# Kernel tuning notes

Measured on AMD Instinct MI355X. Metric: run time of the kernel, lower is better.

## Reference

```python
import jax, jax.numpy as jnp
import numpy as np
from jax.experimental.ode import odeint

RN = 10000   # number of radial grid points (para['rn'])
RM = 200.0   # max radius (para['rm'])
NE = 1000    # number of eigenvalue samples (evl_tr)


def setup_inputs() -> dict:
    # Match the source driver exactly: evl = linspace(-0.05, 1, 1000),
    # r_dsc = linspace(rm/rn, rm, rn).
    evl = jnp.linspace(-0.05, 1.0, NE, dtype=jnp.float32)
    r_dsc = jnp.linspace(RM / RN, RM, RN, dtype=jnp.float32)
    return {"evl": evl, "r_dsc": r_dsc}


def reference(evl, r_dsc):
    E = evl.shape[0]
    # init state: rad = 0, rad' = 1  -> shape [E, 2]
    y0 = jnp.stack([jnp.zeros((E,), evl.dtype), jnp.ones((E,), evl.dtype)], axis=-1)

    def ode_func(y, t, evl):
        rad = y[:, 0]
        rad_d = y[:, 1]
        # ptl_rs = -2/r (Coulomb potential term), broadcast over eigenvalues
        rad_dd = (-2.0 / t - evl) * rad
        return jnp.stack([rad_d, rad_dd], axis=-1)

    # dopri5 adaptive RK45, same tolerances as torchdiffeq call.
    # Output: [RN, E, 2] solution sampled at every r_dsc point.
    return odeint(ode_func, y0, r_dsc, evl, rtol=1e-6, atol=1e-9)
```

## Files before the change

kernel.cpp:

```cpp
#include <hip/hip_runtime.h>

#define NE_  1000
#define RN_  10000
#define NI_  (RN_ - 1)
#define CH_  10
#define NCH_ 1000
#define GL_  25
#define GG_  40

__device__ __forceinline__ float rcpf(float x) { return __builtin_amdgcn_rcpf(x); }

__device__ __forceinline__ void substeps_for(int p, int& S, float& invS) {
    if (p < 16)      { S = 4; invS = 0.25f; }
    else if (p < 64) { S = 2; invS = 0.5f;  }
    else             { S = 1; invS = 1.0f;  }
}

template <int NV>
__device__ __forceinline__ void rk4_step(float q1, float q2, float q3,
                                         float h2, float h, float h6,
                                         float a[NV], float b[NV]) {
#pragma unroll
    for (int v = 0; v < NV; ++v) {
        const float ya = a[v], yb = b[v];
        const float k1a = yb;                const float k1b = q1 * ya;
        const float y2a = fmaf(h2, k1a, ya); const float y2b = fmaf(h2, k1b, yb);
        const float k2a = y2b;               const float k2b = q2 * y2a;
        const float y3a = fmaf(h2, k2a, ya); const float y3b = fmaf(h2, k2b, yb);
        const float k3a = y3b;               const float k3b = q2 * y3a;
        const float y4a = fmaf(h,  k3a, ya); const float y4b = fmaf(h,  k3b, yb);
        const float k4a = y4b;               const float k4b = q3 * y4a;
        a[v] = fmaf(h6, fmaf(2.0f, k2a + k3a, k1a + k4a), ya);
        b[v] = fmaf(h6, fmaf(2.0f, k2b + k3b, k1b + k4b), yb);
    }
}

template <int NV>
__device__ __forceinline__ void advance_interval(float ta, float tb, float e,
                                                 int S, float invS,
                                                 float a[NV], float b[NV]) {
    const float hs = (tb - ta) * invS;
    const float h2 = 0.5f * hs;
    const float h6 = hs * (1.0f / 6.0f);
    for (int j = 0; j < S; ++j) {
        const float t0 = ta + hs * (float)j;
        const float q1 = fmaf(-2.0f, rcpf(t0),      -e);
        const float q2 = fmaf(-2.0f, rcpf(t0 + h2), -e);
        const float q3 = fmaf(-2.0f, rcpf(t0 + hs), -e);
        rk4_step<NV>(q1, q2, q3, h2, hs, h6, a, b);
    }
}

__global__ void k_prop(const float* __restrict__ evl, const float* __restrict__ t,
                       float4* __restrict__ M) {
    const int tid = blockIdx.x * blockDim.x + threadIdx.x;
    if (tid >= NE_ * NCH_) return;
    const int ei = tid % NE_;
    const int c  = tid / NE_;
    const float e    = evl[ei];
    const float t0g  = t[0];
    const float step = (t[RN_ - 1] - t0g) * (1.0f / (float)NI_);
    const int p0 = c * CH_;
    const int p1 = min(p0 + CH_, NI_);
    float a[2] = {1.0f, 0.0f};
    float b[2] = {0.0f, 1.0f};
    if (p0 >= 64 && p0 + CH_ == p1) {
        float tcur = fmaf((float)p0, step, t0g);
        float qcur = fmaf(-2.0f, rcpf(tcur), -e);
#pragma unroll
        for (int k = 0; k < CH_ / 2; ++k) {
            const float pf    = (float)(p0 + 2 * k);
            const float tmid  = fmaf(pf + 1.0f, step, t0g);
            const float tnext = fmaf(pf + 2.0f, step, t0g);
            const float h  = tnext - tcur;
            const float h2 = 0.5f * h;
            const float h6 = h * (1.0f / 6.0f);
            const float qmid  = fmaf(-2.0f, rcpf(tmid),  -e);
            const float qnext = fmaf(-2.0f, rcpf(tnext), -e);
            rk4_step<2>(qcur, qmid, qnext, h2, h, h6, a, b);
            tcur = tnext; qcur = qnext;
        }
    } else {
        for (int p = p0; p < p1; ++p) {
            const float ta = fmaf((float)p,       step, t0g);
            const float tb = fmaf((float)(p + 1), step, t0g);
            int S; float invS; substeps_for(p, S, invS);
            advance_interval<2>(ta, tb, e, S, invS, a, b);
        }
    }
    M[tid] = make_float4(a[0], b[0], a[1], b[1]);
}

__device__ __forceinline__ float4 mmul(float4 B, float4 A) {
    float4 r;
    r.x = fmaf(B.x, A.x, B.z * A.y);
    r.y = fmaf(B.y, A.x, B.w * A.y);
    r.z = fmaf(B.x, A.z, B.z * A.w);
    r.w = fmaf(B.y, A.z, B.w * A.w);
    return r;
}

__global__ void k_group(const float4* __restrict__ M, float4* __restrict__ Mg) {
    const int tid = blockIdx.x * blockDim.x + threadIdx.x;
    if (tid >= NE_ * GG_) return;
    const int ei = tid % NE_;
    const int g  = tid / NE_;
    float4 m[GL_];
#pragma unroll
    for (int k = 0; k < GL_; ++k)
        m[k] = M[(size_t)(g * GL_ + k) * NE_ + ei];
    float4 C = m[0];
#pragma unroll
    for (int k = 1; k < GL_; ++k) C = mmul(m[k], C);
    Mg[(size_t)g * NE_ + ei] = C;
}

__global__ void k_scan_groups(const float4* __restrict__ Mg,
                              float2* __restrict__ Yg) {
    const int ei = blockIdx.x * blockDim.x + threadIdx.x;
    if (ei >= NE_) return;
    float ya = 0.0f, yb = 1.0f;
    for (int g0 = 0; g0 < GG_; g0 += 20) {
        float4 m[20];
#pragma unroll
        for (int k = 0; k < 20; ++k)
            m[k] = Mg[(size_t)(g0 + k) * NE_ + ei];
#pragma unroll
        for (int k = 0; k < 20; ++k) {
            Yg[(size_t)(g0 + k) * NE_ + ei] = make_float2(ya, yb);
            const float na = fmaf(m[k].x, ya, m[k].z * yb);
            const float nb = fmaf(m[k].y, ya, m[k].w * yb);
            ya = na; yb = nb;
        }
    }
}

__global__ void k_expand(const float4* __restrict__ M,
                         const float2* __restrict__ Yg,
                         float2* __restrict__ Yst) {
    const int tid = blockIdx.x * blockDim.x + threadIdx.x;
    if (tid >= NE_ * GG_) return;
    const int ei = tid % NE_;
    const int g  = tid / NE_;
    float4 m[GL_];
#pragma unroll
    for (int k = 0; k < GL_; ++k)
        m[k] = M[(size_t)(g * GL_ + k) * NE_ + ei];
    const float2 y0 = Yg[(size_t)g * NE_ + ei];
    float ya = y0.x, yb = y0.y;
#pragma unroll
    for (int k = 0; k < GL_; ++k) {
        Yst[(size_t)(g * GL_ + k) * NE_ + ei] = make_float2(ya, yb);
        const float na = fmaf(m[k].x, ya, m[k].z * yb);
        const float nb = fmaf(m[k].y, ya, m[k].w * yb);
        ya = na; yb = nb;
    }
}

__global__ void k_out(const float* __restrict__ evl, const float* __restrict__ t,
                      const float2* __restrict__ Yst, float2* __restrict__ out) {
    const int tid = blockIdx.x * blockDim.x + threadIdx.x;
    if (tid >= NE_ * NCH_) return;
    const int ei = tid % NE_;
    const int c  = tid / NE_;
    const float e    = evl[ei];
    const float t0g  = t[0];
    const float step = (t[RN_ - 1] - t0g) * (1.0f / (float)NI_);
    const int p0 = c * CH_;
    const int p1 = min(p0 + CH_, NI_);
    const float2 y0 = Yst[tid];
    float a[1] = {y0.x};
    float b[1] = {y0.y};
    if (c == 0) out[ei] = make_float2(0.0f, 1.0f);
    if (p0 >= 64 && p0 + CH_ == p1) {
        float tcur = fmaf((float)p0, step, t0g);
        float qcur = fmaf(-2.0f, rcpf(tcur), -e);
#pragma unroll
        for (int k = 0; k < CH_; ++k) {
            const float pf    = (float)(p0 + k);
            const float tmid  = fmaf(pf + 0.5f, step, t0g);
            const float tnext = fmaf(pf + 1.0f, step, t0g);
            const float h  = tnext - tcur;
            const float h2 = 0.5f * h;
            const float h6 = h * (1.0f / 6.0f);
            const float qmid  = fmaf(-2.0f, rcpf(tmid),  -e);
            const float qnext = fmaf(-2.0f, rcpf(tnext), -e);
            rk4_step<1>(qcur, qmid, qnext, h2, h, h6, a, b);
            out[(size_t)(p0 + k + 1) * NE_ + ei] = make_float2(a[0], b[0]);
            tcur = tnext; qcur = qnext;
        }
    } else {
        for (int p = p0; p < p1; ++p) {
            const float ta = fmaf((float)p,       step, t0g);
            const float tb = fmaf((float)(p + 1), step, t0g);
            int S; float invS; substeps_for(p, S, invS);
            advance_interval<1>(ta, tb, e, S, invS, a, b);
            out[(size_t)(p + 1) * NE_ + ei] = make_float2(a[0], b[0]);
        }
    }
}

__global__ void k_serial(const float* __restrict__ evl, const float* __restrict__ t,
                         float2* __restrict__ out) {
    const int ei = blockIdx.x * blockDim.x + threadIdx.x;
    if (ei >= NE_) return;
    const float e    = evl[ei];
    const float t0g  = t[0];
    const float step = (t[RN_ - 1] - t0g) * (1.0f / (float)NI_);
    float a[1] = {0.0f};
    float b[1] = {1.0f};
    out[ei] = make_float2(0.0f, 1.0f);
    for (int p = 0; p < NI_; ++p) {
        const float ta = fmaf((float)p,       step, t0g);
        const float tb = fmaf((float)(p + 1), step, t0g);
        int S; float invS; substeps_for(p, S, invS);
        advance_interval<1>(ta, tb, e, S, invS, a, b);
        out[(size_t)(p + 1) * NE_ + ei] = make_float2(a[0], b[0]);
    }
}

extern "C" void kernel_launch(void* const* d_in, const int* in_sizes, int n_in,
                              void* d_out, int out_size, void* d_ws, size_t ws_size,
                              hipStream_t stream) {
    const float* evl = (const float*)d_in[0];
    const float* t   = (const float*)d_in[1];
    float2* out = (float2*)d_out;

    const size_t szM   = (size_t)NCH_ * NE_ * sizeof(float4);
    const size_t szYst = (size_t)NCH_ * NE_ * sizeof(float2);
    const size_t szMg  = (size_t)GG_  * NE_ * sizeof(float4);
    const size_t szYg  = (size_t)GG_  * NE_ * sizeof(float2);

    if (ws_size < szM + szYst + szMg + szYg) {
        k_serial<<<(NE_ + 255) / 256, 256, 0, stream>>>(evl, t, out);
        return;
    }

    char* p = (char*)d_ws;
    float4* M   = (float4*)p;               p += szM;
    float2* Yst = (float2*)p;               p += szYst;
    float4* Mg  = (float4*)p;               p += szMg;
    float2* Yg  = (float2*)p;

    const int ntask   = NE_ * NCH_;
    const int blocks  = (ntask + 255) / 256;
    const int gtask   = NE_ * GG_;
    const int gblocks = (gtask + 255) / 256;

    k_prop<<<blocks, 256, 0, stream>>>(evl, t, M);
    k_group<<<gblocks, 256, 0, stream>>>(M, Mg);
    k_scan_groups<<<4, 256, 0, stream>>>(Mg, Yg);
    k_expand<<<gblocks, 256, 0, stream>>>(M, Yg, Yst);
    k_out<<<blocks, 256, 0, stream>>>(evl, t, Yst, out);
}
```

Baseline: 119.6 us.

## Fuse propagation, group products, scan and expansion into one shared-memory kernel

Replaces four kernels (per-chunk transfer matrices, group products, serial group scan, expansion) with one kernel. Each block handles 8 energies with 64 slots, and each slot computes 16 chunk matrices held in registers. The slot products are scanned in shared memory, and the chunk start states are written straight out. This removes the global round-trip of the full matrix array and three launches. In exchange the kernel uses more registers (16 float4 per thread) and runs a serial 64-step scan in one slot, which may lower occupancy. There are only 125 blocks, which may underfill the GPU.

After: 124.5 us. 4.1% more time.

```diff
diff --git a/kernel.cpp b/kernel.cpp
--- a/kernel.cpp
+++ b/kernel.cpp
@@ -1,12 +1,13 @@
 #include <hip/hip_runtime.h>
 
-#define NE_  1000
-#define RN_  10000
-#define NI_  (RN_ - 1)
-#define CH_  10
-#define NCH_ 1000
-#define GL_  25
-#define GG_  40
+#define NE_    1000
+#define RN_    10000
+#define NI_    (RN_ - 1)
+#define CH_    10
+#define NCH_   1000
+#define SLOTS_ 64
+#define CPS_   16
+#define CPB_   8
 
 __device__ __forceinline__ float rcpf(float x) { return __builtin_amdgcn_rcpf(x); }
 
@@ -51,46 +52,6 @@
     }
 }
 
-__global__ void k_prop(const float* __restrict__ evl, const float* __restrict__ t,
-                       float4* __restrict__ M) {
-    const int tid = blockIdx.x * blockDim.x + threadIdx.x;
-    if (tid >= NE_ * NCH_) return;
-    const int ei = tid % NE_;
-    const int c  = tid / NE_;
-    const float e    = evl[ei];
-    const float t0g  = t[0];
-    const float step = (t[RN_ - 1] - t0g) * (1.0f / (float)NI_);
-    const int p0 = c * CH_;
-    const int p1 = min(p0 + CH_, NI_);
-    float a[2] = {1.0f, 0.0f};
-    float b[2] = {0.0f, 1.0f};
-    if (p0 >= 64 && p0 + CH_ == p1) {
-        float tcur = fmaf((float)p0, step, t0g);
-        float qcur = fmaf(-2.0f, rcpf(tcur), -e);
-#pragma unroll
-        for (int k = 0; k < CH_ / 2; ++k) {
-            const float pf    = (float)(p0 + 2 * k);
-            const float tmid  = fmaf(pf + 1.0f, step, t0g);
-            const float tnext = fmaf(pf + 2.0f, step, t0g);
-            const float h  = tnext - tcur;
-            const float h2 = 0.5f * h;
-            const float h6 = h * (1.0f / 6.0f);
-            const float qmid  = fmaf(-2.0f, rcpf(tmid),  -e);
-            const float qnext = fmaf(-2.0f, rcpf(tnext), -e);
-            rk4_step<2>(qcur, qmid, qnext, h2, h, h6, a, b);
-            tcur = tnext; qcur = qnext;
-        }
-    } else {
-        for (int p = p0; p < p1; ++p) {
-            const float ta = fmaf((float)p,       step, t0g);
-            const float tb = fmaf((float)(p + 1), step, t0g);
-            int S; float invS; substeps_for(p, S, invS);
-            advance_interval<2>(ta, tb, e, S, invS, a, b);
-        }
-    }
-    M[tid] = make_float4(a[0], b[0], a[1], b[1]);
-}
-
 __device__ __forceinline__ float4 mmul(float4 B, float4 A) {
     float4 r;
     r.x = fmaf(B.x, A.x, B.z * A.y);
@@ -100,59 +61,87 @@
     return r;
 }
 
-__global__ void k_group(const float4* __restrict__ M, float4* __restrict__ Mg) {
-    const int tid = blockIdx.x * blockDim.x + threadIdx.x;
-    if (tid >= NE_ * GG_) return;
-    const int ei = tid % NE_;
-    const int g  = tid / NE_;
-    float4 m[GL_];
-#pragma unroll
-    for (int k = 0; k < GL_; ++k)
-        m[k] = M[(size_t)(g * GL_ + k) * NE_ + ei];
-    float4 C = m[0];
-#pragma unroll
-    for (int k = 1; k < GL_; ++k) C = mmul(m[k], C);
-    Mg[(size_t)g * NE_ + ei] = C;
-}
-
-__global__ void k_scan_groups(const float4* __restrict__ Mg,
-                              float2* __restrict__ Yg) {
-    const int ei = blockIdx.x * blockDim.x + threadIdx.x;
-    if (ei >= NE_) return;
-    float ya = 0.0f, yb = 1.0f;
-    for (int g0 = 0; g0 < GG_; g0 += 20) {
-        float4 m[20];
-#pragma unroll
-        for (int k = 0; k < 20; ++k)
-            m[k] = Mg[(size_t)(g0 + k) * NE_ + ei];
-#pragma unroll
-        for (int k = 0; k < 20; ++k) {
-            Yg[(size_t)(g0 + k) * NE_ + ei] = make_float2(ya, yb);
-            const float na = fmaf(m[k].x, ya, m[k].z * yb);
-            const float nb = fmaf(m[k].y, ya, m[k].w * yb);
+__global__ __launch_bounds__(CPB_ * SLOTS_) void
+k_scanfused(const float* __restrict__ evl, const float* __restrict__ t,
+            float2* __restrict__ Yst) {
+    __shared__ float4 lm[CPB_][SLOTS_];
+    __shared__ float2 ly[CPB_][SLOTS_];
+
+    const int tid  = threadIdx.x;
+    const int eil  = tid & (CPB_ - 1);
+    const int slot = tid >> 3;
+    const int ei   = blockIdx.x * CPB_ + eil;
+
+    const float e    = evl[ei];
+    const float t0g  = t[0];
+    const float step = (t[RN_ - 1] - t0g) * (1.0f / (float)NI_);
+
+    float4 Mc[CPS_];
+#pragma unroll
+    for (int i = 0; i < CPS_; ++i) {
+        const int c  = slot * CPS_ + i;
+        const int p0 = c * CH_;
+        const int p1 = min(p0 + CH_, NI_);
+        float a2[2] = {1.0f, 0.0f};
+        float b2[2] = {0.0f, 1.0f};
+        if (p0 < NI_) {
+            if (p0 >= 64 && p1 == p0 + CH_) {
+                float tcur = fmaf((float)p0, step, t0g);
+                float qcur = fmaf(-2.0f, rcpf(tcur), -e);
+#pragma unroll
+                for (int k = 0; k < CH_ / 2; ++k) {
+                    const float pf    = (float)(p0 + 2 * k);
+                    const float tmid  = fmaf(pf + 1.0f, step, t0g);
+                    const float tnext = fmaf(pf + 2.0f, step, t0g);
+                    const float h  = tnext - tcur;
+                    const float h2 = 0.5f * h;
+                    const float h6 = h * (1.0f / 6.0f);
+                    const float qmid  = fmaf(-2.0f, rcpf(tmid),  -e);
+                    const float qnext = fmaf(-2.0f, rcpf(tnext), -e);
+                    rk4_step<2>(qcur, qmid, qnext, h2, h, h6, a2, b2);
+                    tcur = tnext; qcur = qnext;
+                }
+            } else {
+                for (int p = p0; p < p1; ++p) {
+                    const float ta = fmaf((float)p,       step, t0g);
+                    const float tb = fmaf((float)(p + 1), step, t0g);
+                    int S; float invS; substeps_for(p, S, invS);
+                    advance_interval<2>(ta, tb, e, S, invS, a2, b2);
+                }
+            }
+        }
+        Mc[i] = make_float4(a2[0], b2[0], a2[1], b2[1]);
+    }
+
+    float4 C = Mc[0];
+#pragma unroll
+    for (int i = 1; i < CPS_; ++i) C = mmul(Mc[i], C);
+    lm[eil][slot] = C;
+    __syncthreads();
+
+    if (slot == 0) {
+        float ya = 0.0f, yb = 1.0f;
+#pragma unroll 8
+        for (int k = 0; k < SLOTS_; ++k) {
+            ly[eil][k] = make_float2(ya, yb);
+            const float4 m = lm[eil][k];
+            const float na = fmaf(m.x, ya, m.z * yb);
+            const float nb = fmaf(m.y, ya, m.w * yb);
             ya = na; yb = nb;
         }
     }
-}
-
-__global__ void k_expand(const float4* __restrict__ M,
-                         const float2* __restrict__ Yg,
-                         float2* __restrict__ Yst) {
-    const int tid = blockIdx.x * blockDim.x + threadIdx.x;
-    if (tid >= NE_ * GG_) return;
-    const int ei = tid % NE_;
-    const int g  = tid / NE_;
-    float4 m[GL_];
-#pragma unroll
-    for (int k = 0; k < GL_; ++k)
-        m[k] = M[(size_t)(g * GL_ + k) * NE_ + ei];
-    const float2 y0 = Yg[(size_t)g * NE_ + ei];
+    __syncthreads();
+
+    const float2 y0 = ly[eil][slot];
     float ya = y0.x, yb = y0.y;
 #pragma unroll
-    for (int k = 0; k < GL_; ++k) {
-        Yst[(size_t)(g * GL_ + k) * NE_ + ei] = make_float2(ya, yb);
-        const float na = fmaf(m[k].x, ya, m[k].z * yb);
-        const float nb = fmaf(m[k].y, ya, m[k].w * yb);
+    for (int i = 0; i < CPS_; ++i) {
+        const int c = slot * CPS_ + i;
+        if (c < NCH_)
+            Yst[(size_t)c * NE_ + ei] = make_float2(ya, yb);
+        const float4 m = Mc[i];
+        const float na = fmaf(m.x, ya, m.z * yb);
+        const float nb = fmaf(m.y, ya, m.w * yb);
         ya = na; yb = nb;
     }
 }
@@ -226,30 +215,14 @@
     const float* t   = (const float*)d_in[1];
     float2* out = (float2*)d_out;
 
-    const size_t szM   = (size_t)NCH_ * NE_ * sizeof(float4);
-    const size_t szYst = (size_t)NCH_ * NE_ * sizeof(float2);
-    const size_t szMg  = (size_t)GG_  * NE_ * sizeof(float4);
-    const size_t szYg  = (size_t)GG_  * NE_ * sizeof(float2);
-
-    if (ws_size < szM + szYst + szMg + szYg) {
+    const size_t needYst = (size_t)NCH_ * NE_ * sizeof(float2);
+    if (ws_size < needYst) {
         k_serial<<<(NE_ + 255) / 256, 256, 0, stream>>>(evl, t, out);
         return;
     }
-
-    char* p = (char*)d_ws;
-    float4* M   = (float4*)p;               p += szM;
-    float2* Yst = (float2*)p;               p += szYst;
-    float4* Mg  = (float4*)p;               p += szMg;
-    float2* Yg  = (float2*)p;
-
-    const int ntask   = NE_ * NCH_;
-    const int blocks  = (ntask + 255) / 256;
-    const int gtask   = NE_ * GG_;
-    const int gblocks = (gtask + 255) / 256;
-
-    k_prop<<<blocks, 256, 0, stream>>>(evl, t, M);
-    k_group<<<gblocks, 256, 0, stream>>>(M, Mg);
-    k_scan_groups<<<4, 256, 0, stream>>>(Mg, Yg);
-    k_expand<<<gblocks, 256, 0, stream>>>(M, Yg, Yst);
-    k_out<<<blocks, 256, 0, stream>>>(evl, t, Yst, out);
-}
+    float2* Yst = (float2*)d_ws;
+
+    k_scanfused<<<NE_ / CPB_, CPB_ * SLOTS_, 0, stream>>>(evl, t, Yst);
+    const int ntask = NE_ * NCH_;
+    k_out<<<(ntask + 255) / 256, 256, 0, stream>>>(evl, t, Yst, out);
+}
```

## Merge group scan into expand and use wider RK4 steps in prop

Applied to the files above, without the earlier changes.

Removes the single-wave k_scan_groups launch. Each expand thread now recomputes its own group prefix by applying all earlier group matrices directly, which trades one launch and a serial dependency for redundant reads and FMAs of Mg. Separately, the fast path of k_prop now takes three RK4 steps of widths 4, 4 and 2 grid intervals instead of five steps of width 2. This cuts the arithmetic in that path but raises the per-step truncation error, so accuracy may suffer.

New measurement: 117.1 us. 1.02x faster.

```diff
diff --git a/kernel.cpp b/kernel.cpp
--- a/kernel.cpp
+++ b/kernel.cpp
@@ -67,18 +67,20 @@
     if (p0 >= 64 && p0 + CH_ == p1) {
         float tcur = fmaf((float)p0, step, t0g);
         float qcur = fmaf(-2.0f, rcpf(tcur), -e);
-#pragma unroll
-        for (int k = 0; k < CH_ / 2; ++k) {
-            const float pf    = (float)(p0 + 2 * k);
-            const float tmid  = fmaf(pf + 1.0f, step, t0g);
-            const float tnext = fmaf(pf + 2.0f, step, t0g);
+        int p = p0;
+        const int widths[3] = {4, 4, 2};
+#pragma unroll
+        for (int s = 0; s < 3; ++s) {
+            const int w = widths[s];
+            const float tmid  = fmaf((float)(p + w / 2), step, t0g);
+            const float tnext = fmaf((float)(p + w),     step, t0g);
             const float h  = tnext - tcur;
             const float h2 = 0.5f * h;
             const float h6 = h * (1.0f / 6.0f);
             const float qmid  = fmaf(-2.0f, rcpf(tmid),  -e);
             const float qnext = fmaf(-2.0f, rcpf(tnext), -e);
             rk4_step<2>(qcur, qmid, qnext, h2, h, h6, a, b);
-            tcur = tnext; qcur = qnext;
+            tcur = tnext; qcur = qnext; p += w;
         }
     } else {
         for (int p = p0; p < p1; ++p) {
@@ -115,39 +117,35 @@
     Mg[(size_t)g * NE_ + ei] = C;
 }
 
-__global__ void k_scan_groups(const float4* __restrict__ Mg,
-                              float2* __restrict__ Yg) {
-    const int ei = blockIdx.x * blockDim.x + threadIdx.x;
-    if (ei >= NE_) return;
+__global__ void k_expand(const float4* __restrict__ M,
+                         const float4* __restrict__ Mg,
+                         float2* __restrict__ Yst) {
+    const int tid = blockIdx.x * blockDim.x + threadIdx.x;
+    if (tid >= NE_ * GG_) return;
+    const int ei = tid % NE_;
+    const int g  = tid / NE_;
+
     float ya = 0.0f, yb = 1.0f;
-    for (int g0 = 0; g0 < GG_; g0 += 20) {
-        float4 m[20];
-#pragma unroll
-        for (int k = 0; k < 20; ++k)
-            m[k] = Mg[(size_t)(g0 + k) * NE_ + ei];
-#pragma unroll
-        for (int k = 0; k < 20; ++k) {
-            Yg[(size_t)(g0 + k) * NE_ + ei] = make_float2(ya, yb);
-            const float na = fmaf(m[k].x, ya, m[k].z * yb);
-            const float nb = fmaf(m[k].y, ya, m[k].w * yb);
-            ya = na; yb = nb;
-        }
-    }
-}
-
-__global__ void k_expand(const float4* __restrict__ M,
-                         const float2* __restrict__ Yg,
-                         float2* __restrict__ Yst) {
-    const int tid = blockIdx.x * blockDim.x + threadIdx.x;
-    if (tid >= NE_ * GG_) return;
-    const int ei = tid % NE_;
-    const int g  = tid / NE_;
+    for (int j0 = 0; j0 < GG_; j0 += 8) {
+        if (j0 >= g) break;
+        float4 mm[8];
+#pragma unroll
+        for (int k = 0; k < 8; ++k)
+            mm[k] = Mg[(size_t)(j0 + k) * NE_ + ei];
+#pragma unroll
+        for (int k = 0; k < 8; ++k) {
+            if (j0 + k < g) {
+                const float na = fmaf(mm[k].x, ya, mm[k].z * yb);
+                const float nb = fmaf(mm[k].y, ya, mm[k].w * yb);
+                ya = na; yb = nb;
+            }
+        }
+    }
+
     float4 m[GL_];
 #pragma unroll
     for (int k = 0; k < GL_; ++k)
         m[k] = M[(size_t)(g * GL_ + k) * NE_ + ei];
-    const float2 y0 = Yg[(size_t)g * NE_ + ei];
-    float ya = y0.x, yb = y0.y;
 #pragma unroll
     for (int k = 0; k < GL_; ++k) {
         Yst[(size_t)(g * GL_ + k) * NE_ + ei] = make_float2(ya, yb);
@@ -229,9 +227,8 @@
     const size_t szM   = (size_t)NCH_ * NE_ * sizeof(float4);
     const size_t szYst = (size_t)NCH_ * NE_ * sizeof(float2);
     const size_t szMg  = (size_t)GG_  * NE_ * sizeof(float4);
-    const size_t szYg  = (size_t)GG_  * NE_ * sizeof(float2);
-
-    if (ws_size < szM + szYst + szMg + szYg) {
+
+    if (ws_size < szM + szYst + szMg) {
         k_serial<<<(NE_ + 255) / 256, 256, 0, stream>>>(evl, t, out);
         return;
     }
@@ -239,8 +236,7 @@
     char* p = (char*)d_ws;
     float4* M   = (float4*)p;               p += szM;
     float2* Yst = (float2*)p;               p += szYst;
-    float4* Mg  = (float4*)p;               p += szMg;
-    float2* Yg  = (float2*)p;
+    float4* Mg  = (float4*)p;
 
     const int ntask   = NE_ * NCH_;
     const int blocks  = (ntask + 255) / 256;
@@ -249,7 +245,6 @@
 
     k_prop<<<blocks, 256, 0, stream>>>(evl, t, M);
     k_group<<<gblocks, 256, 0, stream>>>(M, Mg);
-    k_scan_groups<<<4, 256, 0, stream>>>(Mg, Yg);
-    k_expand<<<gblocks, 256, 0, stream>>>(M, Yg, Yst);
+    k_expand<<<gblocks, 256, 0, stream>>>(M, Mg, Yst);
     k_out<<<blocks, 256, 0, stream>>>(evl, t, Yst, out);
 }
```
